# Kernel tuning notes

Measured on AMD Instinct MI355X. Metric: run time of the kernel, lower is better.

## Reference

```python
import jax, jax.numpy as jnp
import numpy as np

B, S, D = 2, 2048, 1024
H = 16
DK = D // H


def setup_inputs() -> dict:
    key = jax.random.key(0)
    ks = jax.random.split(key, 5)
    std = np.sqrt(2.0 / (D + D))
    x = jax.random.normal(ks[0], (B, S, D), dtype=jnp.float32)
    wq = jax.random.normal(ks[1], (D, D), dtype=jnp.float32) * std
    wk = jax.random.normal(ks[2], (D, D), dtype=jnp.float32) * std
    wv = jax.random.normal(ks[3], (D, D), dtype=jnp.float32) * std
    wo = jax.random.normal(ks[4], (D, D), dtype=jnp.float32) * std
    return {"x": x, "wq": wq, "wk": wk, "wv": wv, "wo": wo}


def reference(x, wq, wk, wv, wo):
    # Linear: y = x @ W.T  (weight stored as [d_out, d_in])
    q = jnp.einsum("bsd,ed->bse", x, wq)
    k = jnp.einsum("bsd,ed->bse", x, wk)
    v = jnp.einsum("bsd,ed->bse", x, wv)
    # split heads: [B, S, H*DK] -> [B, H, S, DK]
    q = q.reshape(B, S, H, DK).transpose(0, 2, 1, 3)
    k = k.reshape(B, S, H, DK).transpose(0, 2, 1, 3)
    v = v.reshape(B, S, H, DK).transpose(0, 2, 1, 3)
    scale = 1.0 / jnp.sqrt(jnp.asarray(DK, dtype=x.dtype))
    scores = jnp.einsum("bhqd,bhkd->bhqk", q, k) * scale  # [B,H,S,S]
    causal = jnp.tril(jnp.ones((S, S), dtype=bool))
    scores = jnp.where(causal, scores, -jnp.inf)
    attn = jax.nn.softmax(scores, axis=-1)
    out = jnp.einsum("bhqk,bhkd->bhqd", attn, v)  # [B,H,S,DK]
    out = out.transpose(0, 2, 1, 3).reshape(B, S, D)
    return jnp.einsum("bsd,ed->bse", out, wo)
```

## Files before the change

kernel.cpp:

```cpp
#include <hip/hip_runtime.h>
#include <hip/hip_bf16.h>
#include <cstdint>

#define B_ 2
#define S_ 2048
#define D_ 1024
#define H_ 16
#define DK_ 64

typedef __attribute__((ext_vector_type(8))) short bf16x8;
typedef __attribute__((ext_vector_type(4))) float f32x4;

__device__ __forceinline__ unsigned short f2bf(float f) {
  unsigned u = __float_as_uint(f);
  u = (u + 0x7FFFu + ((u >> 16) & 1u)) >> 16;
  return (unsigned short)u;
}

typedef __attribute__((address_space(1))) void gv_t;
typedef __attribute__((address_space(3))) void lv_t;
__device__ __forceinline__ void gl16(const void* g, void* l) {
  __builtin_amdgcn_global_load_lds((gv_t*)g, (lv_t*)l, 16, 0, 0);
}

__device__ __forceinline__ void stage8w(const unsigned short* gbase, size_t ldg,
                                        unsigned short* lds, int wave, int lane) {
  const int lr = lane >> 3;
  const int col8 = (lane & 7) ^ lr;
  gl16(gbase + (size_t)(wave * 8 + lr) * ldg + col8 * 8, lds + wave * 512);
}

__device__ __forceinline__ bf16x8 rdswz(const unsigned short* lds, int row, int col) {
  return *(const bf16x8*)&lds[row * 64 + (col ^ ((row & 7) << 3))];
}

__global__ void cvt_kernel(const float* __restrict__ in, unsigned short* __restrict__ out, int n4) {
  int i = blockIdx.x * blockDim.x + threadIdx.x;
  if (i >= n4) return;
  const float4 v = reinterpret_cast<const float4*>(in)[i];
  ushort4 o;
  o.x = f2bf(v.x); o.y = f2bf(v.y); o.z = f2bf(v.z); o.w = f2bf(v.w);
  reinterpret_cast<ushort4*>(out)[i] = o;
}

__global__ void cvtw_kernel(const float* __restrict__ w0, const float* __restrict__ w1,
                            const float* __restrict__ w2, const float* __restrict__ w3,
                            unsigned short* __restrict__ o0, unsigned short* __restrict__ o1,
                            unsigned short* __restrict__ o2, unsigned short* __restrict__ o3) {
  const int mat = blockIdx.y;
  const float* in = (mat == 0) ? w0 : (mat == 1) ? w1 : (mat == 2) ? w2 : w3;
  unsigned short* out = (mat == 0) ? o0 : (mat == 1) ? o1 : (mat == 2) ? o2 : o3;
  int i = blockIdx.x * blockDim.x + threadIdx.x;
  const float4 v = reinterpret_cast<const float4*>(in)[i];
  ushort4 o;
  o.x = f2bf(v.x); o.y = f2bf(v.y); o.z = f2bf(v.z); o.w = f2bf(v.w);
  reinterpret_cast<ushort4*>(out)[i] = o;
}

#define BM 128
#define BK 64

template <typename OutT, bool TV2, int BNv>
__global__ __launch_bounds__(256) void gemm_bt(
    const unsigned short* __restrict__ A,
    const unsigned short* __restrict__ B0, const unsigned short* __restrict__ B1,
    const unsigned short* __restrict__ B2,
    OutT* __restrict__ C0, OutT* __restrict__ C1, OutT* __restrict__ C2,
    int M, int N, int K) {
  constexpr int NFRAG = BNv / 32;
  __shared__ unsigned short lA[BM * BK];
  __shared__ unsigned short lB[BNv * BK];
  const int tid = threadIdx.x;
  const int wave = tid >> 6, lane = tid & 63;
  const int l16 = lane & 15, lqq = lane >> 4;
  const int wr = wave >> 1, wc = wave & 1;
  const int lr = lane >> 3;
  const int col8 = ((lane & 7) ^ lr) * 8;

  const int tilesPerMat = N / BNv;
  const int bx = blockIdx.x;
  const int mat = bx / tilesPerMat;
  const int n0 = (bx % tilesPerMat) * BNv;
  const unsigned short* Bm = (mat == 0) ? B0 : (mat == 1) ? B1 : B2;
  OutT* C = (mat == 0) ? C0 : (mat == 1) ? C1 : C2;
  const int m0 = blockIdx.y * BM;

  f32x4 acc[4][NFRAG] = {};

  for (int k0 = 0; k0 < K; k0 += BK) {
    __syncthreads();
#pragma unroll
    for (int c = wave; c < 16; c += 4)
      gl16(A + (size_t)(m0 + c * 8 + lr) * K + k0 + col8, &lA[c * 512]);
#pragma unroll
    for (int c = wave; c < BNv / 8; c += 4)
      gl16(Bm + (size_t)(n0 + c * 8 + lr) * K + k0 + col8, &lB[c * 512]);
    __syncthreads();
#pragma unroll
    for (int kk = 0; kk < BK / 32; ++kk) {
      bf16x8 af[4], bfr[NFRAG];
#pragma unroll
      for (int m = 0; m < 4; ++m)
        af[m] = rdswz(lA, wr * 64 + m * 16 + l16, kk * 32 + lqq * 8);
#pragma unroll
      for (int n = 0; n < NFRAG; ++n)
        bfr[n] = rdswz(lB, wc * (BNv / 2) + n * 16 + l16, kk * 32 + lqq * 8);
      __builtin_amdgcn_s_setprio(1);
#pragma unroll
      for (int m = 0; m < 4; ++m)
#pragma unroll
        for (int n = 0; n < NFRAG; ++n)
          acc[m][n] = __builtin_amdgcn_mfma_f32_16x16x32_bf16(af[m], bfr[n], acc[m][n], 0, 0, 0);
      __builtin_amdgcn_s_setprio(0);
    }
  }

  if (TV2 && mat == 2) {
    unsigned short* Vt = (unsigned short*)C;
#pragma unroll
    for (int m = 0; m < 4; ++m)
#pragma unroll
      for (int n = 0; n < NFRAG; ++n) {
        int r0 = m0 + wr * 64 + m * 16 + lqq * 4;
        int cidx = n0 + wc * (BNv / 2) + n * 16 + l16;
        int bb = r0 >> 11, s = r0 & 2047;
        int h = cidx >> 6, dv = cidx & 63;
        ushort4 o;
        o.x = f2bf(acc[m][n][0]); o.y = f2bf(acc[m][n][1]);
        o.z = f2bf(acc[m][n][2]); o.w = f2bf(acc[m][n][3]);
        *(ushort4*)(Vt + ((size_t)((bb * H_ + h) * DK_ + dv)) * S_ + s) = o;
      }
  } else {
#pragma unroll
    for (int m = 0; m < 4; ++m)
#pragma unroll
      for (int n = 0; n < NFRAG; ++n)
#pragma unroll
        for (int j = 0; j < 4; ++j) {
          int r = m0 + wr * 64 + m * 16 + lqq * 4 + j;
          int cidx = n0 + wc * (BNv / 2) + n * 16 + l16;
          float v = acc[m][n][j];
          if constexpr (sizeof(OutT) == 4) C[(size_t)r * N + cidx] = v;
          else C[(size_t)r * N + cidx] = f2bf(v);
        }
  }
}

__global__ __launch_bounds__(512) void attn_kernel(
    const unsigned short* __restrict__ Qg, const unsigned short* __restrict__ Kg,
    const unsigned short* __restrict__ Vtg, unsigned short* __restrict__ Og) {
  __shared__ unsigned short sQ[2][64 * 64];
  __shared__ unsigned short sK[2][64 * 64];
  __shared__ unsigned short sVt[2][64 * 64];
  __shared__ unsigned short sP[8][2][16 * 64];
  const int tid = threadIdx.x, wave = tid >> 6, lane = tid & 63;
  const int side = wave >> 2, wq = wave & 3;
  const int l16 = lane & 15, lq = lane >> 4;
  const int id = blockIdx.x;
  const int bh = (id & 7) * 4 + ((id >> 3) & 3);
  const int g = (id >> 5) & 7;
  const int i = (id < 256) ? (15 - g) : g;
  const int b = bh >> 4, h = bh & 15;
  const int qtA = 2 * i, qtB = 2 * i + 1;
  const int qt_s = side ? qtB : qtA;
  const int NT = i + 1;
  const size_t tokbase = (size_t)b * S_ * D_ + h * DK_;
  const unsigned short* VtB = Vtg + (size_t)(b * H_ + h) * DK_ * S_;
  unsigned short (*sPw)[16 * 64] = sP[wave];

  stage8w(Qg + tokbase + (size_t)(qtA * 64) * D_, D_, sQ[0], wave, lane);
  stage8w(Qg + tokbase + (size_t)(qtB * 64) * D_, D_, sQ[1], wave, lane);
  __syncthreads();
  bf16x8 aq0 = rdswz(sQ[side], wq * 16 + l16, lq * 8);
  bf16x8 aq1 = rdswz(sQ[side], wq * 16 + l16, 32 + lq * 8);

  const float LOG2E_S = 0.125f * 1.44269504f;
  const float THR2 = 11.5416f;
  float m_run[4] = {-1e30f, -1e30f, -1e30f, -1e30f};
  float l_run[4] = {0.f, 0.f, 0.f, 0.f};
  f32x4 o_acc[4] = {};

#pragma unroll 1
  for (int kt = 0; kt < NT; ++kt) {
    __syncthreads();
    stage8w(Kg + tokbase + (size_t)(kt * 128) * D_, D_, sK[0], wave, lane);
    stage8w(Kg + tokbase + (size_t)(kt * 128 + 64) * D_, D_, sK[1], wave, lane);
    stage8w(VtB + kt * 128, S_, sVt[0], wave, lane);
    stage8w(VtB + kt * 128 + 64, S_, sVt[1], wave, lane);
    __syncthreads();

    const bool last = (kt == NT - 1);
    float p[8][4];

#pragma unroll
    for (int sub = 0; sub < 2; ++sub) {
      const bool skip = (sub == 1) && (side == 0) && last;
      if (!skip) {
        __builtin_amdgcn_s_setprio(1);
#pragma unroll
        for (int nb = 0; nb < 4; ++nb) {
          bf16x8 bk0 = rdswz(sK[sub], nb * 16 + l16, lq * 8);
          bf16x8 bk1 = rdswz(sK[sub], nb * 16 + l16, 32 + lq * 8);
          f32x4 a = {};
          a = __builtin_amdgcn_mfma_f32_16x16x32_bf16(aq0, bk0, a, 0, 0, 0);
          a = __builtin_amdgcn_mfma_f32_16x16x32_bf16(aq1, bk1, a, 0, 0, 0);
#pragma unroll
          for (int j = 0; j < 4; ++j) p[sub * 4 + nb][j] = a[j] * LOG2E_S;
        }
        __builtin_amdgcn_s_setprio(0);
      } else {
#pragma unroll
        for (int nb = 0; nb < 4; ++nb)
#pragma unroll
          for (int j = 0; j < 4; ++j) p[sub * 4 + nb][j] = -1e30f;
      }
    }

    if (last) {
      if (side == 0) {
#pragma unroll
        for (int nb = 0; nb < 4; ++nb)
#pragma unroll
          for (int j = 0; j < 4; ++j) {
            int kidx = nb * 16 + l16;
            int qidx = wq * 16 + lq * 4 + j;
            if (kidx > qidx) p[nb][j] = -1e30f;
          }
      } else {
#pragma unroll
        for (int nb = 0; nb < 4; ++nb)
#pragma unroll
          for (int j = 0; j < 4; ++j) {
            int kidx = nb * 16 + l16;
            int qidx = wq * 16 + lq * 4 + j;
            if (kidx > qidx) p[4 + nb][j] = -1e30f;
          }
      }
    }

    float pmax[4];
    bool ok = true;
#pragma unroll
    for (int j = 0; j < 4; ++j) {
      float r = p[0][j];
#pragma unroll
      for (int nbb = 1; nbb < 8; ++nbb) r = fmaxf(r, p[nbb][j]);
      pmax[j] = r;
      ok = ok && (r <= m_run[j] + THR2);
    }
    if (!__all((int)ok)) {
#pragma unroll
      for (int j = 0; j < 4; ++j) {
        float r = pmax[j];
#pragma unroll
        for (int d = 1; d < 16; d <<= 1) r = fmaxf(r, __shfl_xor(r, d));
        float mn = fmaxf(m_run[j], r);
        float alpha = exp2f(m_run[j] - mn);
        m_run[j] = mn;
        l_run[j] *= alpha;
#pragma unroll
        for (int nb = 0; nb < 4; ++nb) o_acc[nb][j] *= alpha;
      }
    }
#pragma unroll
    for (int j = 0; j < 4; ++j) {
      const int rw = lq * 4 + j;
#pragma unroll
      for (int nbb = 0; nbb < 8; ++nbb) {
        float e = exp2f(p[nbb][j] - m_run[j]);
        l_run[j] += e;
        sPw[nbb >> 2][rw * 64 + (((nbb & 3) * 16 + l16) ^ ((rw & 7) << 3))] = f2bf(e);
      }
    }

    __builtin_amdgcn_s_setprio(1);
#pragma unroll
    for (int sub = 0; sub < 2; ++sub)
#pragma unroll
      for (int kk = 0; kk < 2; ++kk) {
        bf16x8 ap = rdswz(sPw[sub], l16, kk * 32 + lq * 8);
#pragma unroll
        for (int nb = 0; nb < 4; ++nb) {
          bf16x8 bv = rdswz(sVt[sub], nb * 16 + l16, kk * 32 + lq * 8);
          o_acc[nb] = __builtin_amdgcn_mfma_f32_16x16x32_bf16(ap, bv, o_acc[nb], 0, 0, 0);
        }
      }
    __builtin_amdgcn_s_setprio(0);
  }

#pragma unroll
  for (int j = 0; j < 4; ++j) {
    float s = l_run[j];
#pragma unroll
    for (int d = 1; d < 16; d <<= 1) s += __shfl_xor(s, d);
    float inv = 1.f / s;
#pragma unroll
    for (int nb = 0; nb < 4; ++nb) {
      int r = qt_s * 64 + wq * 16 + lq * 4 + j;
      Og[tokbase + (size_t)r * D_ + nb * 16 + l16] = f2bf(o_acc[nb][j] * inv);
    }
  }
}

extern "C" void kernel_launch(void* const* d_in, const int* in_sizes, int n_in,
                              void* d_out, int out_size, void* d_ws, size_t ws_size,
                              hipStream_t stream) {
  const float* x = (const float*)d_in[0];
  const float* wq = (const float*)d_in[1];
  const float* wk = (const float*)d_in[2];
  const float* wv = (const float*)d_in[3];
  const float* wo = (const float*)d_in[4];
  float* out = (float*)d_out;

  char* ws = (char*)d_ws;
  const size_t MB = 1024 * 1024;
  unsigned short* xb  = (unsigned short*)(ws + 0);
  unsigned short* wqb = (unsigned short*)(ws + 8 * MB);
  unsigned short* wkb = (unsigned short*)(ws + 10 * MB);
  unsigned short* wvb = (unsigned short*)(ws + 12 * MB);
  unsigned short* wob = (unsigned short*)(ws + 14 * MB);
  unsigned short* Qb  = (unsigned short*)(ws + 16 * MB);
  unsigned short* Kb  = (unsigned short*)(ws + 24 * MB);
  unsigned short* Vtb = (unsigned short*)(ws + 32 * MB);
  unsigned short* AOb = (unsigned short*)(ws + 40 * MB);

  const int M = B_ * S_;
  const int N = D_, K = D_;

  cvt_kernel<<<dim3((M * D_ / 4 + 255) / 256), 256, 0, stream>>>(x, xb, M * D_ / 4);
  cvtw_kernel<<<dim3(D_ * D_ / 4 / 256, 4), 256, 0, stream>>>(wq, wk, wv, wo, wqb, wkb, wvb, wob);

  gemm_bt<unsigned short, true, 128><<<dim3(3 * (N / 128), M / BM), 256, 0, stream>>>(
      xb, wqb, wkb, wvb, Qb, Kb, Vtb, M, N, K);

  attn_kernel<<<dim3(512), 512, 0, stream>>>(Qb, Kb, Vtb, AOb);

  gemm_bt<float, false, 64><<<dim3(N / 64, M / BM), 256, 0, stream>>>(
      AOb, wob, wob, wob, out, out, out, M, N, K);
}
```

Measured before the change: 121.0 us.

## Double-buffer K/V tiles in attention and merge conversion kernels into one launch

The attention loop now walks 64-key tiles instead of 128-key tiles. It prefetches the next K and V^T tile into a second LDS buffer while computing on the current one, and uses one barrier per iteration instead of two. Waves for the lower query tile skip work past their diagonal rather than filling masked scores. The separate x and weight fp32-to-bf16 conversion kernels are merged into a single 2D launch, removing one kernel launch at the cost of many idle blocks in the weight rows. The risk is that halving the tile doubles the loop iterations and barriers, and side-0 waves sit idle at barriers on the final iteration.

```diff
diff --git a/kernel.cpp b/kernel.cpp
--- a/kernel.cpp
+++ b/kernel.cpp
@@ -34,23 +34,18 @@
   return *(const bf16x8*)&lds[row * 64 + (col ^ ((row & 7) << 3))];
 }
 
-__global__ void cvt_kernel(const float* __restrict__ in, unsigned short* __restrict__ out, int n4) {
+__global__ void cvt_all_kernel(const float* __restrict__ x,
+                               const float* __restrict__ w0, const float* __restrict__ w1,
+                               const float* __restrict__ w2, const float* __restrict__ w3,
+                               unsigned short* __restrict__ xo,
+                               unsigned short* __restrict__ o0, unsigned short* __restrict__ o1,
+                               unsigned short* __restrict__ o2, unsigned short* __restrict__ o3) {
+  const int mat = blockIdx.y;
+  const float* in = (mat == 0) ? x : (mat == 1) ? w0 : (mat == 2) ? w1 : (mat == 3) ? w2 : w3;
+  unsigned short* out = (mat == 0) ? xo : (mat == 1) ? o0 : (mat == 2) ? o1 : (mat == 3) ? o2 : o3;
+  const int n4 = (mat == 0) ? (B_ * S_ * D_ / 4) : (D_ * D_ / 4);
   int i = blockIdx.x * blockDim.x + threadIdx.x;
   if (i >= n4) return;
-  const float4 v = reinterpret_cast<const float4*>(in)[i];
-  ushort4 o;
-  o.x = f2bf(v.x); o.y = f2bf(v.y); o.z = f2bf(v.z); o.w = f2bf(v.w);
-  reinterpret_cast<ushort4*>(out)[i] = o;
-}
-
-__global__ void cvtw_kernel(const float* __restrict__ w0, const float* __restrict__ w1,
-                            const float* __restrict__ w2, const float* __restrict__ w3,
-                            unsigned short* __restrict__ o0, unsigned short* __restrict__ o1,
-                            unsigned short* __restrict__ o2, unsigned short* __restrict__ o3) {
-  const int mat = blockIdx.y;
-  const float* in = (mat == 0) ? w0 : (mat == 1) ? w1 : (mat == 2) ? w2 : w3;
-  unsigned short* out = (mat == 0) ? o0 : (mat == 1) ? o1 : (mat == 2) ? o2 : o3;
-  int i = blockIdx.x * blockDim.x + threadIdx.x;
   const float4 v = reinterpret_cast<const float4*>(in)[i];
   ushort4 o;
   o.x = f2bf(v.x); o.y = f2bf(v.y); o.z = f2bf(v.z); o.w = f2bf(v.w);
@@ -152,7 +147,7 @@
   __shared__ unsigned short sQ[2][64 * 64];
   __shared__ unsigned short sK[2][64 * 64];
   __shared__ unsigned short sVt[2][64 * 64];
-  __shared__ unsigned short sP[8][2][16 * 64];
+  __shared__ unsigned short sP[8][16 * 64];
   const int tid = threadIdx.x, wave = tid >> 6, lane = tid & 63;
   const int side = wave >> 2, wq = wave & 3;
   const int l16 = lane & 15, lq = lane >> 4;
@@ -163,13 +158,15 @@
   const int b = bh >> 4, h = bh & 15;
   const int qtA = 2 * i, qtB = 2 * i + 1;
   const int qt_s = side ? qtB : qtA;
-  const int NT = i + 1;
+  const int NT = qtB + 1;
   const size_t tokbase = (size_t)b * S_ * D_ + h * DK_;
   const unsigned short* VtB = Vtg + (size_t)(b * H_ + h) * DK_ * S_;
-  unsigned short (*sPw)[16 * 64] = sP[wave];
+  unsigned short* sPw = sP[wave];
 
   stage8w(Qg + tokbase + (size_t)(qtA * 64) * D_, D_, sQ[0], wave, lane);
   stage8w(Qg + tokbase + (size_t)(qtB * 64) * D_, D_, sQ[1], wave, lane);
+  stage8w(Kg + tokbase, D_, sK[0], wave, lane);
+  stage8w(VtB, S_, sVt[0], wave, lane);
   __syncthreads();
   bf16x8 aq0 = rdswz(sQ[side], wq * 16 + l16, lq * 8);
   bf16x8 aq1 = rdswz(sQ[side], wq * 16 + l16, 32 + lq * 8);
@@ -182,42 +179,28 @@
 
 #pragma unroll 1
   for (int kt = 0; kt < NT; ++kt) {
-    __syncthreads();
-    stage8w(Kg + tokbase + (size_t)(kt * 128) * D_, D_, sK[0], wave, lane);
-    stage8w(Kg + tokbase + (size_t)(kt * 128 + 64) * D_, D_, sK[1], wave, lane);
-    stage8w(VtB + kt * 128, S_, sVt[0], wave, lane);
-    stage8w(VtB + kt * 128 + 64, S_, sVt[1], wave, lane);
-    __syncthreads();
-
-    const bool last = (kt == NT - 1);
-    float p[8][4];
-
-#pragma unroll
-    for (int sub = 0; sub < 2; ++sub) {
-      const bool skip = (sub == 1) && (side == 0) && last;
-      if (!skip) {
-        __builtin_amdgcn_s_setprio(1);
-#pragma unroll
-        for (int nb = 0; nb < 4; ++nb) {
-          bf16x8 bk0 = rdswz(sK[sub], nb * 16 + l16, lq * 8);
-          bf16x8 bk1 = rdswz(sK[sub], nb * 16 + l16, 32 + lq * 8);
-          f32x4 a = {};
-          a = __builtin_amdgcn_mfma_f32_16x16x32_bf16(aq0, bk0, a, 0, 0, 0);
-          a = __builtin_amdgcn_mfma_f32_16x16x32_bf16(aq1, bk1, a, 0, 0, 0);
-#pragma unroll
-          for (int j = 0; j < 4; ++j) p[sub * 4 + nb][j] = a[j] * LOG2E_S;
-        }
-        __builtin_amdgcn_s_setprio(0);
-      } else {
-#pragma unroll
-        for (int nb = 0; nb < 4; ++nb)
-#pragma unroll
-          for (int j = 0; j < 4; ++j) p[sub * 4 + nb][j] = -1e30f;
-      }
+    const int cur = kt & 1;
+    if (kt + 1 < NT) {
+      stage8w(Kg + tokbase + (size_t)((kt + 1) * 64) * D_, D_, sK[cur ^ 1], wave, lane);
+      stage8w(VtB + (kt + 1) * 64, S_, sVt[cur ^ 1], wave, lane);
     }
 
-    if (last) {
-      if (side == 0) {
+    if (side || kt <= qtA) {
+      float p[4][4];
+      __builtin_amdgcn_s_setprio(1);
+#pragma unroll
+      for (int nb = 0; nb < 4; ++nb) {
+        bf16x8 bk0 = rdswz(sK[cur], nb * 16 + l16, lq * 8);
+        bf16x8 bk1 = rdswz(sK[cur], nb * 16 + l16, 32 + lq * 8);
+        f32x4 a = {};
+        a = __builtin_amdgcn_mfma_f32_16x16x32_bf16(aq0, bk0, a, 0, 0, 0);
+        a = __builtin_amdgcn_mfma_f32_16x16x32_bf16(aq1, bk1, a, 0, 0, 0);
+#pragma unroll
+        for (int j = 0; j < 4; ++j) p[nb][j] = a[j] * LOG2E_S;
+      }
+      __builtin_amdgcn_s_setprio(0);
+
+      if (kt == qt_s) {
 #pragma unroll
         for (int nb = 0; nb < 4; ++nb)
 #pragma unroll
@@ -226,66 +209,55 @@
             int qidx = wq * 16 + lq * 4 + j;
             if (kidx > qidx) p[nb][j] = -1e30f;
           }
-      } else {
-#pragma unroll
-        for (int nb = 0; nb < 4; ++nb)
-#pragma unroll
-          for (int j = 0; j < 4; ++j) {
-            int kidx = nb * 16 + l16;
-            int qidx = wq * 16 + lq * 4 + j;
-            if (kidx > qidx) p[4 + nb][j] = -1e30f;
-          }
-      }
-    }
-
-    float pmax[4];
-    bool ok = true;
-#pragma unroll
-    for (int j = 0; j < 4; ++j) {
-      float r = p[0][j];
-#pragma unroll
-      for (int nbb = 1; nbb < 8; ++nbb) r = fmaxf(r, p[nbb][j]);
-      pmax[j] = r;
-      ok = ok && (r <= m_run[j] + THR2);
-    }
-    if (!__all((int)ok)) {
+      }
+
+      float pmax[4];
+      bool ok = true;
 #pragma unroll
       for (int j = 0; j < 4; ++j) {
-        float r = pmax[j];
-#pragma unroll
-        for (int d = 1; d < 16; d <<= 1) r = fmaxf(r, __shfl_xor(r, d));
-        float mn = fmaxf(m_run[j], r);
-        float alpha = exp2f(m_run[j] - mn);
-        m_run[j] = mn;
-        l_run[j] *= alpha;
-#pragma unroll
-        for (int nb = 0; nb < 4; ++nb) o_acc[nb][j] *= alpha;
-      }
-    }
-#pragma unroll
-    for (int j = 0; j < 4; ++j) {
-      const int rw = lq * 4 + j;
-#pragma unroll
-      for (int nbb = 0; nbb < 8; ++nbb) {
-        float e = exp2f(p[nbb][j] - m_run[j]);
-        l_run[j] += e;
-        sPw[nbb >> 2][rw * 64 + (((nbb & 3) * 16 + l16) ^ ((rw & 7) << 3))] = f2bf(e);
-      }
-    }
-
-    __builtin_amdgcn_s_setprio(1);
-#pragma unroll
-    for (int sub = 0; sub < 2; ++sub)
+        float r = fmaxf(fmaxf(p[0][j], p[1][j]), fmaxf(p[2][j], p[3][j]));
+        pmax[j] = r;
+        ok = ok && (r <= m_run[j] + THR2);
+      }
+      if (!__all((int)ok)) {
+#pragma unroll
+        for (int j = 0; j < 4; ++j) {
+          float r = pmax[j];
+#pragma unroll
+          for (int d = 1; d < 16; d <<= 1) r = fmaxf(r, __shfl_xor(r, d));
+          float mn = fmaxf(m_run[j], r);
+          float alpha = exp2f(m_run[j] - mn);
+          m_run[j] = mn;
+          l_run[j] *= alpha;
+#pragma unroll
+          for (int nb = 0; nb < 4; ++nb) o_acc[nb][j] *= alpha;
+        }
+      }
+#pragma unroll
+      for (int j = 0; j < 4; ++j) {
+        const int rw = lq * 4 + j;
+#pragma unroll
+        for (int nb = 0; nb < 4; ++nb) {
+          float e = exp2f(p[nb][j] - m_run[j]);
+          l_run[j] += e;
+          sPw[rw * 64 + (((nb * 16 + l16) ^ ((rw & 7) << 3)))] = f2bf(e);
+        }
+      }
+
+      __builtin_amdgcn_s_setprio(1);
 #pragma unroll
       for (int kk = 0; kk < 2; ++kk) {
-        bf16x8 ap = rdswz(sPw[sub], l16, kk * 32 + lq * 8);
+        bf16x8 ap = rdswz(sPw, l16, kk * 32 + lq * 8);
 #pragma unroll
         for (int nb = 0; nb < 4; ++nb) {
-          bf16x8 bv = rdswz(sVt[sub], nb * 16 + l16, kk * 32 + lq * 8);
+          bf16x8 bv = rdswz(sVt[cur], nb * 16 + l16, kk * 32 + lq * 8);
           o_acc[nb] = __builtin_amdgcn_mfma_f32_16x16x32_bf16(ap, bv, o_acc[nb], 0, 0, 0);
         }
       }
-    __builtin_amdgcn_s_setprio(0);
+      __builtin_amdgcn_s_setprio(0);
+    }
+
+    __syncthreads();
   }
 
 #pragma unroll
@@ -327,8 +299,8 @@
   const int M = B_ * S_;
   const int N = D_, K = D_;
 
-  cvt_kernel<<<dim3((M * D_ / 4 + 255) / 256), 256, 0, stream>>>(x, xb, M * D_ / 4);
-  cvtw_kernel<<<dim3(D_ * D_ / 4 / 256, 4), 256, 0, stream>>>(wq, wk, wv, wo, wqb, wkb, wvb, wob);
+  cvt_all_kernel<<<dim3(B_ * S_ * D_ / 4 / 256, 5), 256, 0, stream>>>(
+      x, wq, wk, wv, wo, xb, wqb, wkb, wvb, wob);
 
   gemm_bt<unsigned short, true, 128><<<dim3(3 * (N / 128), M / BM), 256, 0, stream>>>(
       xb, wqb, wkb, wvb, Qb, Kb, Vtb, M, N, K);
```

Result: slower. 124.2 us (+2.6%).
